# Performance work log

Hardware: AMD Instinct MI355X
Metric: run time of the kernel (lower is better)

## Reference

```python
import jax, jax.numpy as jnp
import numpy as np

_W = jnp.array([10., 9., 8., 7., 6., 5., 4., 3., 2., 1.], dtype=jnp.float32)
_W_NORM = _W / jnp.sum(_W)  # np.average normalizes by weight sum (55)


def setup_inputs() -> dict:
    key = jax.random.key(0)
    k1, k2 = jax.random.split(key)
    x = jax.random.randint(k1, (1024, 64, 10), 0, 8000, dtype=jnp.int32)
    table = jax.random.normal(k2, (8000, 256), dtype=jnp.float32)
    return {"x": x, "table": table}


def reference(x, table):
    # Gather per-char vectors: [T, F, 10, D]
    vecs = table[x]
    # Weighted average over the 10 chars (weights [10..1], normalized)
    return jnp.einsum('tfcd,c->tfd', vecs, _W_NORM)
```

## Files before the change

### kernel.cpp

```cpp
#include <hip/hip_runtime.h>
#include <hip/hip_fp16.h>


#define ROWS_TOTAL (1024 * 64)
#define TROWS 8000
#define TD 256

typedef float v4f __attribute__((ext_vector_type(4)));
typedef _Float16 h8 __attribute__((ext_vector_type(8)));

__global__ __launch_bounds__(256)
void cvt_perm2(const float* __restrict__ t, _Float16* __restrict__ o) {
    const int tid = blockIdx.x * 256 + threadIdx.x;
    const int row = tid >> 5;
    const int s   = (tid >> 4) & 1;
    const int i   = tid & 15;
    const float* src = t + (size_t)row * TD + s * 128 + 4 * i;
    v4f a = *reinterpret_cast<const v4f*>(src);
    v4f b = *reinterpret_cast<const v4f*>(src + 64);
    h8 r;
    r[0] = (_Float16)a.x; r[1] = (_Float16)a.y;
    r[2] = (_Float16)a.z; r[3] = (_Float16)a.w;
    r[4] = (_Float16)b.x; r[5] = (_Float16)b.y;
    r[6] = (_Float16)b.z; r[7] = (_Float16)b.w;
    __builtin_nontemporal_store(r, reinterpret_cast<h8*>(o + (size_t)tid * 8));
}

__global__ __launch_bounds__(256)
void char2vec_w2(const int* __restrict__ x,
                 const _Float16* __restrict__ tb,
                 float* __restrict__ out) {
    const int l  = threadIdx.x & 63;
    const int wv = threadIdx.x >> 6;
    const int q  = l >> 4;
    const int i  = l & 15;

    const int s       = blockIdx.x & 1;
    const int rowbase = (blockIdx.x >> 1) * 16 + wv * 4;
    const int row     = rowbase + q;

    const int t = x[rowbase * 10 + (l < 40 ? l : 39)];

    int idx[10];
#pragma unroll
    for (int c = 0; c < 10; ++c) idx[c] = __shfl(t, q * 10 + c);

    h8 v[10];
#pragma unroll
    for (int c = 0; c < 10; ++c)
        v[c] = *reinterpret_cast<const h8*>(
            tb + (size_t)idx[c] * TD + s * 128 + i * 8);

    const float w[10] = {10.f / 55.f, 9.f / 55.f, 8.f / 55.f, 7.f / 55.f,
                         6.f / 55.f,  5.f / 55.f, 4.f / 55.f, 3.f / 55.f,
                         2.f / 55.f,  1.f / 55.f};

    float acc[8] = {0, 0, 0, 0, 0, 0, 0, 0};
#pragma unroll
    for (int c = 0; c < 10; ++c) {
#pragma unroll
        for (int e = 0; e < 8; ++e)
            acc[e] = fmaf((float)v[c][e], w[c], acc[e]);
    }

    v4f lo = {acc[0], acc[1], acc[2], acc[3]};
    v4f hi = {acc[4], acc[5], acc[6], acc[7]};
    float* orow = out + (size_t)row * TD + s * 128;
    *reinterpret_cast<v4f*>(orow + 4 * i)      = lo;
    *reinterpret_cast<v4f*>(orow + 64 + 4 * i) = hi;
}

__global__ __launch_bounds__(256)
void char2vec_sliced2(const int* __restrict__ x,
                      const float* __restrict__ table,
                      float* __restrict__ out) {
    const int slice = blockIdx.x & 7;
    const int rgrp  = blockIdx.x >> 3;
    const int wave  = threadIdx.x >> 6;
    const int lane  = threadIdx.x & 63;

    const int row0 = rgrp * 64 + wave * 16 + (lane >> 3) * 2;
    const int row1 = row0 + 1;
    const int d    = slice * 32 + (lane & 7) * 4;

    const int2* __restrict__ xa = reinterpret_cast<const int2*>(x + row0 * 10);
    const int2* __restrict__ xb = reinterpret_cast<const int2*>(x + row1 * 10);
    int2 pa[5], pb[5];
#pragma unroll
    for (int i = 0; i < 5; ++i) pa[i] = xa[i];
#pragma unroll
    for (int i = 0; i < 5; ++i) pb[i] = xb[i];

    int ia[10], ib[10];
#pragma unroll
    for (int i = 0; i < 5; ++i) {
        ia[2 * i] = pa[i].x; ia[2 * i + 1] = pa[i].y;
        ib[2 * i] = pb[i].x; ib[2 * i + 1] = pb[i].y;
    }

    v4f va[10], vb[10];
#pragma unroll
    for (int c = 0; c < 10; ++c)
        va[c] = *reinterpret_cast<const v4f*>(table + (size_t)ia[c] * TD + d);
#pragma unroll
    for (int c = 0; c < 10; ++c)
        vb[c] = *reinterpret_cast<const v4f*>(table + (size_t)ib[c] * TD + d);

    const float w[10] = {10.f / 55.f, 9.f / 55.f, 8.f / 55.f, 7.f / 55.f,
                         6.f / 55.f,  5.f / 55.f, 4.f / 55.f, 3.f / 55.f,
                         2.f / 55.f,  1.f / 55.f};

    v4f acc0 = (v4f)0.0f, acc1 = (v4f)0.0f;
#pragma unroll
    for (int c = 0; c < 10; ++c) {
        acc0 += va[c] * w[c];
        acc1 += vb[c] * w[c];
    }

    __builtin_nontemporal_store(
        acc0, reinterpret_cast<v4f*>(out + (size_t)row0 * TD + d));
    __builtin_nontemporal_store(
        acc1, reinterpret_cast<v4f*>(out + (size_t)row1 * TD + d));
}

extern "C" void kernel_launch(void* const* d_in, const int* in_sizes, int n_in,
                              void* d_out, int out_size, void* d_ws, size_t ws_size,
                              hipStream_t stream) {
    const int*   x     = (const int*)d_in[0];
    const float* table = (const float*)d_in[1];
    float*       out   = (float*)d_out;

    const size_t f16_bytes = (size_t)TROWS * TD * sizeof(_Float16);

    if (ws_size >= f16_bytes) {
        _Float16* tb = (_Float16*)d_ws;
        cvt_perm2<<<(TROWS * 32) / 256, 256, 0, stream>>>(table, tb);
        char2vec_w2<<<(ROWS_TOTAL / 16) * 2, 256, 0, stream>>>(x, tb, out);
    } else {
        const int blocks = (ROWS_TOTAL / 64) * 8;
        char2vec_sliced2<<<blocks, 256, 0, stream>>>(x, table, out);
    }
}
```

Before: 29.59 us.

## Fuse table conversion and gather into one cooperative persistent kernel

Replaces the two back-to-back launches (fp32-to-fp16 table conversion, then gather and weighted sum) with a single cooperative kernel. It converts the table in a grid-stride loop, performs a grid-wide sync, then loops persistently over the gather work. This is meant to remove the second launch overhead and the gap between kernels. In exchange it adds a grid barrier, an occupancy query on every call, and a persistent grid sized at up to 1024 blocks; if the cooperative launch fails it falls back to the old two-kernel path.

```diff
diff --git a/kernel.cpp b/kernel.cpp
--- a/kernel.cpp
+++ b/kernel.cpp
@@ -1,13 +1,97 @@
 #include <hip/hip_runtime.h>
 #include <hip/hip_fp16.h>
+#include <hip/hip_cooperative_groups.h>
 
 
 #define ROWS_TOTAL (1024 * 64)
 #define TROWS 8000
 #define TD 256
+#define VBLKS 8192
 
 typedef float v4f __attribute__((ext_vector_type(4)));
 typedef _Float16 h8 __attribute__((ext_vector_type(8)));
+
+namespace cg = cooperative_groups;
+
+__device__ __forceinline__ void cvt_chunk(const float* __restrict__ table,
+                                          _Float16* __restrict__ tb,
+                                          int c, int p) {
+    const int row = c >> 4;
+    const int i   = c & 15;
+    const float* src = table + (size_t)row * TD + p * 128 + 4 * i;
+    v4f a = *reinterpret_cast<const v4f*>(src);
+    v4f b = *reinterpret_cast<const v4f*>(src + 64);
+    h8 r;
+    r[0] = (_Float16)a.x; r[1] = (_Float16)a.y;
+    r[2] = (_Float16)a.z; r[3] = (_Float16)a.w;
+    r[4] = (_Float16)b.x; r[5] = (_Float16)b.y;
+    r[6] = (_Float16)b.z; r[7] = (_Float16)b.w;
+    __builtin_nontemporal_store(
+        r, reinterpret_cast<h8*>(tb + ((size_t)row * 32 + p * 16 + i) * 8));
+}
+
+__device__ __forceinline__ void main_body(const int* __restrict__ x,
+                                          const _Float16* __restrict__ tb,
+                                          float* __restrict__ out,
+                                          int vb, int l, int wv) {
+    const int q = l >> 4;
+    const int i = l & 15;
+    const int s       = vb & 1;
+    const int rowbase = (vb >> 1) * 16 + wv * 4;
+    const int row     = rowbase + q;
+
+    const int t = x[rowbase * 10 + (l < 40 ? l : 39)];
+
+    int idx[10];
+#pragma unroll
+    for (int c = 0; c < 10; ++c) idx[c] = __shfl(t, q * 10 + c);
+
+    h8 v[10];
+#pragma unroll
+    for (int c = 0; c < 10; ++c)
+        v[c] = *reinterpret_cast<const h8*>(
+            tb + (size_t)idx[c] * TD + s * 128 + i * 8);
+
+    const float w[10] = {10.f / 55.f, 9.f / 55.f, 8.f / 55.f, 7.f / 55.f,
+                         6.f / 55.f,  5.f / 55.f, 4.f / 55.f, 3.f / 55.f,
+                         2.f / 55.f,  1.f / 55.f};
+
+    float acc[8] = {0, 0, 0, 0, 0, 0, 0, 0};
+#pragma unroll
+    for (int c = 0; c < 10; ++c) {
+#pragma unroll
+        for (int e = 0; e < 8; ++e)
+            acc[e] = fmaf((float)v[c][e], w[c], acc[e]);
+    }
+
+    v4f lo = {acc[0], acc[1], acc[2], acc[3]};
+    v4f hi = {acc[4], acc[5], acc[6], acc[7]};
+    float* orow = out + (size_t)row * TD + s * 128;
+    *reinterpret_cast<v4f*>(orow + 4 * i)      = lo;
+    *reinterpret_cast<v4f*>(orow + 64 + 4 * i) = hi;
+}
+
+__global__ __launch_bounds__(256, 2)
+void char2vec_coop(const int* __restrict__ x,
+                   const float* __restrict__ table,
+                   _Float16* __restrict__ tb,
+                   float* __restrict__ out) {
+    const int p      = blockIdx.x & 1;
+    const int halfId = blockIdx.x >> 1;
+    const int nhalf  = gridDim.x >> 1;
+
+    for (int c = halfId * 256 + (int)threadIdx.x; c < TROWS * 16;
+         c += nhalf * 256)
+        cvt_chunk(table, tb, c, p);
+
+    cg::this_grid().sync();
+
+    const int l  = threadIdx.x & 63;
+    const int wv = threadIdx.x >> 6;
+#pragma unroll 1
+    for (int vb = blockIdx.x; vb < VBLKS; vb += gridDim.x)
+        main_body(x, tb, out, vb, l, wv);
+}
 
 __global__ __launch_bounds__(256)
 void cvt_perm2(const float* __restrict__ t, _Float16* __restrict__ o) {
@@ -15,6 +99,7 @@
     const int row = tid >> 5;
     const int s   = (tid >> 4) & 1;
     const int i   = tid & 15;
+    if (row >= TROWS) return;
     const float* src = t + (size_t)row * TD + s * 128 + 4 * i;
     v4f a = *reinterpret_cast<const v4f*>(src);
     v4f b = *reinterpret_cast<const v4f*>(src + 64);
@@ -32,42 +117,7 @@
                  float* __restrict__ out) {
     const int l  = threadIdx.x & 63;
     const int wv = threadIdx.x >> 6;
-    const int q  = l >> 4;
-    const int i  = l & 15;
-
-    const int s       = blockIdx.x & 1;
-    const int rowbase = (blockIdx.x >> 1) * 16 + wv * 4;
-    const int row     = rowbase + q;
-
-    const int t = x[rowbase * 10 + (l < 40 ? l : 39)];
-
-    int idx[10];
-#pragma unroll
-    for (int c = 0; c < 10; ++c) idx[c] = __shfl(t, q * 10 + c);
-
-    h8 v[10];
-#pragma unroll
-    for (int c = 0; c < 10; ++c)
-        v[c] = *reinterpret_cast<const h8*>(
-            tb + (size_t)idx[c] * TD + s * 128 + i * 8);
-
-    const float w[10] = {10.f / 55.f, 9.f / 55.f, 8.f / 55.f, 7.f / 55.f,
-                         6.f / 55.f,  5.f / 55.f, 4.f / 55.f, 3.f / 55.f,
-                         2.f / 55.f,  1.f / 55.f};
-
-    float acc[8] = {0, 0, 0, 0, 0, 0, 0, 0};
-#pragma unroll
-    for (int c = 0; c < 10; ++c) {
-#pragma unroll
-        for (int e = 0; e < 8; ++e)
-            acc[e] = fmaf((float)v[c][e], w[c], acc[e]);
-    }
-
-    v4f lo = {acc[0], acc[1], acc[2], acc[3]};
-    v4f hi = {acc[4], acc[5], acc[6], acc[7]};
-    float* orow = out + (size_t)row * TD + s * 128;
-    *reinterpret_cast<v4f*>(orow + 4 * i)      = lo;
-    *reinterpret_cast<v4f*>(orow + 64 + 4 * i) = hi;
+    main_body(x, tb, out, blockIdx.x, l, wv);
 }
 
 __global__ __launch_bounds__(256)
@@ -117,10 +167,8 @@
         acc1 += vb[c] * w[c];
     }
 
-    __builtin_nontemporal_store(
-        acc0, reinterpret_cast<v4f*>(out + (size_t)row0 * TD + d));
-    __builtin_nontemporal_store(
-        acc1, reinterpret_cast<v4f*>(out + (size_t)row1 * TD + d));
+    *reinterpret_cast<v4f*>(out + (size_t)row0 * TD + d) = acc0;
+    *reinterpret_cast<v4f*>(out + (size_t)row1 * TD + d) = acc1;
 }
 
 extern "C" void kernel_launch(void* const* d_in, const int* in_sizes, int n_in,
@@ -134,8 +182,34 @@
 
     if (ws_size >= f16_bytes) {
         _Float16* tb = (_Float16*)d_ws;
-        cvt_perm2<<<(TROWS * 32) / 256, 256, 0, stream>>>(table, tb);
-        char2vec_w2<<<(ROWS_TOTAL / 16) * 2, 256, 0, stream>>>(x, tb, out);
+
+        int occ = 0;
+        hipError_t qerr = hipOccupancyMaxActiveBlocksPerMultiprocessor(
+            &occ, char2vec_coop, 256, 0);
+        int nblk = 0;
+        if (qerr == hipSuccess && occ > 0) {
+            long long cand = (long long)occ * 256;
+            if (cand > 1024) cand = 1024;
+            nblk = (int)(cand & ~7LL);
+        }
+
+        bool done = false;
+        if (nblk >= 16) {
+            void* args[4] = {(void*)&x, (void*)&table, (void*)&tb, (void*)&out};
+            hipError_t e = hipLaunchCooperativeKernel(
+                (const void*)char2vec_coop, dim3(nblk), dim3(256), args, 0,
+                stream);
+            if (e == hipSuccess) {
+                done = true;
+            } else {
+                (void)hipGetLastError();
+            }
+        }
+
+        if (!done) {
+            cvt_perm2<<<(TROWS * 32 + 255) / 256, 256, 0, stream>>>(table, tb);
+            char2vec_w2<<<VBLKS, 256, 0, stream>>>(x, tb, out);
+        }
     } else {
         const int blocks = (ROWS_TOTAL / 64) * 8;
         char2vec_sliced2<<<blocks, 256, 0, stream>>>(x, table, out);
```

After: 89.68 us. 3.03x slower.
